# Kernel optimization log

Measured on AMD Instinct MI355X. Metric: run time of the kernel, lower is better.

Reference implementation:

```python
import jax, jax.numpy as jnp
import numpy as np

BN_EPS = 1e-5
DIST_EPS = 1e-8
K = 3  # fixed 3-NN interpolation


def _cond_conv(x, t_embed, w_t, b_t, w_c, b_c, gamma, beta):
    # time conditioning: GELU(t) -> Linear -> add to channels
    te = jax.nn.gelu(t_embed, approximate=False) @ w_t.T + b_t  # (B, Cin)
    x = x + te[:, :, None]
    # kernel-size-1 Conv1d == channel GEMM
    x = jnp.einsum('oc,bcn->bon', w_c, x) + b_c[None, :, None]
    # BatchNorm1d, training mode: biased stats over (batch, length)
    m = jnp.mean(x, axis=(0, 2), keepdims=True)
    v = jnp.var(x, axis=(0, 2), keepdims=True)
    x = gamma[None, :, None] * (x - m) * jax.lax.rsqrt(v + BN_EPS) + beta[None, :, None]
    return jax.nn.gelu(x, approximate=False)


def _forward(xyz1, xyz2, points1, points2, t_embed,
             w_t1, b_t1, w_c1, b_c1, g1, be1,
             w_t2, b_t2, w_c2, b_c2, g2, be2):
    # squared euclidean distances (cdist**2), computed directly
    # d2[b,n,s] = ||xyz1[b,n]||^2 + ||xyz2[b,s]||^2 - 2 <xyz1[b,n], xyz2[b,s]>
    n1 = jnp.sum(xyz1 * xyz1, axis=-1)  # (B,N)
    n2 = jnp.sum(xyz2 * xyz2, axis=-1)  # (B,S)
    d2 = n1[:, :, None] + n2[:, None, :] - 2.0 * jnp.einsum('bnc,bsc->bns', xyz1, xyz2)
    # top-3 smallest distances (instead of wasteful full sort)
    neg, idx = jax.lax.top_k(-d2, K)        # (B,N,3)
    dists = -neg
    dist_recip = 1.0 / (dists + DIST_EPS)
    weight = dist_recip / jnp.sum(dist_recip, axis=2, keepdims=True)  # (B,N,3)
    pts2t = jnp.transpose(points2, (0, 2, 1))  # (B,S,C2)
    gathered = jax.vmap(lambda p, i: p[i])(pts2t, idx)  # (B,N,3,C2)
    interp = jnp.einsum('bnkc,bnk->bcn', gathered, weight)  # (B,C2,N)
    new_points = jnp.concatenate([points1, interp], axis=1)  # (B,C1+C2,N)
    new_points = _cond_conv(new_points, t_embed, w_t1, b_t1, w_c1, b_c1, g1, be1)
    new_points = _cond_conv(new_points, t_embed, w_t2, b_t2, w_c2, b_c2, g2, be2)
    return new_points


def setup_inputs() -> dict:
    key = jax.random.key(0)
    ks = jax.random.split(key, 12)
    B, N, S, C1, C2, T = 8, 8192, 2048, 128, 256, 256
    Cin = C1 + C2
    s = lambda fan: 1.0 / np.sqrt(fan)
    return {
        'xyz1': jax.random.normal(ks[0], (B, N, 3), jnp.float32),
        'xyz2': jax.random.normal(ks[1], (B, S, 3), jnp.float32),
        'points1': jax.random.normal(ks[2], (B, C1, N), jnp.float32),
        'points2': jax.random.normal(ks[3], (B, C2, S), jnp.float32),
        't_embed': jax.random.normal(ks[4], (B, T), jnp.float32),
        'w_t1': jax.random.normal(ks[5], (Cin, T), jnp.float32) * s(T),
        'b_t1': jnp.zeros((Cin,), jnp.float32),
        'w_c1': jax.random.normal(ks[6], (256, Cin), jnp.float32) * s(Cin),
        'b_c1': jnp.zeros((256,), jnp.float32),
        'g1': jnp.ones((256,), jnp.float32),
        'be1': jnp.zeros((256,), jnp.float32),
        'w_t2': jax.random.normal(ks[7], (256, T), jnp.float32) * s(T),
        'b_t2': jnp.zeros((256,), jnp.float32),
        'w_c2': jax.random.normal(ks[8], (256, 256), jnp.float32) * s(256),
        'b_c2': jnp.zeros((256,), jnp.float32),
        'g2': jnp.ones((256,), jnp.float32),
        'be2': jnp.zeros((256,), jnp.float32),
    }


def reference(xyz1, xyz2, points1, points2, t_embed,
              w_t1, b_t1, w_c1, b_c1, g1, be1,
              w_t2, b_t2, w_c2, b_c2, g2, be2):
    return _forward(xyz1, xyz2, points1, points2, t_embed,
                    w_t1, b_t1, w_c1, b_c1, g1, be1,
                    w_t2, b_t2, w_c2, b_c2, g2, be2)
```

## Files before the change

kernel.cpp:

```cpp
#include <hip/hip_runtime.h>
#include <cfloat>
#include <cmath>

#define B_   8
#define N_   8192
#define S_   2048
#define C1_  128
#define C2_  256
#define T_   256
#define CIN_ 384
#define CO_  256

#define KCH  8
#define KCS  (S_ / KCH)
#define KQB  512

typedef __attribute__((ext_vector_type(8))) short short8;
typedef __attribute__((ext_vector_type(4))) float f32x4;

__device__ __forceinline__ float bf2f(unsigned short u) {
    union { unsigned int i; float f; } v; v.i = ((unsigned int)u) << 16; return v.f;
}
__device__ __forceinline__ unsigned short f2bf(float f) {
    union { float f; unsigned int i; } v; v.f = f;
    unsigned int i = v.i;
    unsigned int r = i + 0x7FFFu + ((i >> 16) & 1u);
    return (unsigned short)(r >> 16);
}
__device__ __forceinline__ float gelu_f(float x) {
    return 0.5f * x * (1.0f + erff(x * 0.70710678118654752440f));
}
__device__ __forceinline__ void async16(const void* g, void* l) {
    __builtin_amdgcn_global_load_lds((const __attribute__((address_space(1))) void*)g,
                                     (__attribute__((address_space(3))) void*)l, 16, 0, 0);
}
__device__ __forceinline__ float med3f(float a, float b, float c) {
    float r;
    asm("v_med3_f32 %0, %1, %2, %3" : "=v"(r) : "v"(a), "v"(b), "v"(c));
    return r;
}

#define OFF_TE1   0u
#define OFF_TE2   16384u
#define OFF_BN1   28672u
#define OFF_BN2   30720u
#define OFF_WC1   1605632u
#define OFF_WC2   1802240u
#define OFF_P2T   2097152u
#define OFF_X1    10485760u
#define OFF_Y     60817408u
#define OFF_PD    OFF_Y
#define OFF_PI    (OFF_Y + 6291456u)
#define OFF_PS    OFF_P2T
#define OFF_PQ    (OFF_P2T + 1048576u)

__global__ __launch_bounds__(256) void prep_kernel(
    const float* __restrict__ w1, const float* __restrict__ w2,
    unsigned short* __restrict__ o1, unsigned short* __restrict__ o2,
    const float* __restrict__ t_embed,
    const float* __restrict__ w_t1, const float* __restrict__ b_t1,
    const float* __restrict__ w_t2, const float* __restrict__ b_t2,
    float* __restrict__ te1, float* __restrict__ te2)
{
    int bx = blockIdx.x, t = threadIdx.x;
    if (bx < 384) {
        int g = bx * 256 + t;
        o1[g] = f2bf(w1[g]);
        if (g < CO_ * CO_) o2[g] = f2bf(w2[g]);
        return;
    }
    __shared__ float gt[T_];
    int b = bx - 384;
    gt[t] = gelu_f(t_embed[b * T_ + t]);
    __syncthreads();
    for (int o = t; o < CIN_ + CO_; o += 256) {
        if (o < CIN_) {
            const float* w = w_t1 + o * T_;
            float s = 0.f;
            for (int k = 0; k < T_; ++k) s += gt[k] * w[k];
            te1[b * CIN_ + o] = s + b_t1[o];
        } else {
            int oo = o - CIN_;
            const float* w = w_t2 + oo * T_;
            float s = 0.f;
            for (int k = 0; k < T_; ++k) s += gt[k] * w[k];
            te2[b * CO_ + oo] = s + b_t2[oo];
        }
    }
}

__global__ __launch_bounds__(256) void knn_part_kernel(
    const float* __restrict__ xyz1, const float* __restrict__ xyz2,
    float* __restrict__ pd, int* __restrict__ pi)
{
    __shared__ float4 sp[KCS];
    int b = blockIdx.z, ch = blockIdx.y, tid = threadIdx.x;
    int s0 = ch * KCS;
    {
        int gs = s0 + tid;
        float x = xyz2[(b * S_ + gs) * 3 + 0];
        float y = xyz2[(b * S_ + gs) * 3 + 1];
        float z = xyz2[(b * S_ + gs) * 3 + 2];
        sp[tid] = make_float4(x, y, z, x * x + y * y + z * z);
    }
    __syncthreads();

    float nx[2], ny[2], nz[2], nn[2];
    float d1[2], d2[2], d3[2];
    int   i1[2], i2[2], i3[2];
    #pragma unroll
    for (int qq = 0; qq < 2; ++qq) {
        int n = blockIdx.x * KQB + qq * 256 + tid;
        float x1 = xyz1[(b * N_ + n) * 3 + 0];
        float y1 = xyz1[(b * N_ + n) * 3 + 1];
        float z1 = xyz1[(b * N_ + n) * 3 + 2];
        nn[qq] = x1 * x1 + y1 * y1 + z1 * z1;
        nx[qq] = -2.0f * x1; ny[qq] = -2.0f * y1; nz[qq] = -2.0f * z1;
        d1[qq] = FLT_MAX; d2[qq] = FLT_MAX; d3[qq] = FLT_MAX;
        i1[qq] = 0; i2[qq] = 0; i3[qq] = 0;
    }

    for (int s = 0; s < KCS; s += 4) {
        #pragma unroll
        for (int u = 0; u < 4; ++u) {
            float4 p = sp[s + u];
            int gi = s0 + s + u;
            #pragma unroll
            for (int qq = 0; qq < 2; ++qq) {
                float d = fmaf(nx[qq], p.x,
                          fmaf(ny[qq], p.y,
                          fmaf(nz[qq], p.z, p.w)));
                bool c1 = d < d1[qq];
                bool c2 = d < d2[qq];
                bool c3 = d < d3[qq];
                float e1 = fminf(d1[qq], d);
                float e2 = med3f(d1[qq], d2[qq], d);
                float e3 = med3f(d2[qq], d3[qq], d);
                int u1  = c1 ? i1[qq] : gi;
                int n1i = c1 ? gi : i1[qq];
                int n2i = c2 ? u1 : i2[qq];
                int u2  = c2 ? i2[qq] : gi;
                int n3i = c3 ? u2 : i3[qq];
                d1[qq] = e1; d2[qq] = e2; d3[qq] = e3;
                i1[qq] = n1i; i2[qq] = n2i; i3[qq] = n3i;
            }
        }
    }

    #pragma unroll
    for (int qq = 0; qq < 2; ++qq) {
        int n = blockIdx.x * KQB + qq * 256 + tid;
        size_t pb = (((size_t)b * KCH + ch) * N_ + n) * 3;
        pd[pb + 0] = d1[qq] + nn[qq];
        pd[pb + 1] = d2[qq] + nn[qq];
        pd[pb + 2] = d3[qq] + nn[qq];
        pi[pb + 0] = i1[qq]; pi[pb + 1] = i2[qq]; pi[pb + 2] = i3[qq];
    }
}

__global__ __launch_bounds__(256) void transpose_fused(
    const float* __restrict__ p2, unsigned short* __restrict__ p2t,
    const float* __restrict__ p1, const float* __restrict__ te1,
    unsigned short* __restrict__ X1)
{
    __shared__ unsigned short tile[32][33];
    int bx = blockIdx.x;
    if (bx < 4096) {
        int b = bx >> 9, cy = (bx >> 6) & 7, sx = bx & 63;
        int s0 = sx * 32, c0 = cy * 32;
        #pragma unroll
        for (int j = 0; j < 4; ++j) {
            int c = threadIdx.y + j * 8;
            tile[c][threadIdx.x] = f2bf(p2[((size_t)b * C2_ + c0 + c) * S_ + s0 + threadIdx.x]);
        }
        __syncthreads();
        #pragma unroll
        for (int j = 0; j < 4; ++j) {
            int s = threadIdx.y + j * 8;
            p2t[((size_t)b * S_ + s0 + s) * C2_ + c0 + threadIdx.x] = tile[threadIdx.x][s];
        }
    } else {
        int bz = bx - 4096;
        int b = bz >> 10, cy = (bz >> 8) & 3, nx = bz & 255;
        int n0 = nx * 32, c0 = cy * 32;
        const float* te = te1 + b * CIN_;
        #pragma unroll
        for (int j = 0; j < 4; ++j) {
            int c = threadIdx.y + j * 8;
            tile[c][threadIdx.x] =
                f2bf(p1[((size_t)b * C1_ + c0 + c) * N_ + n0 + threadIdx.x] + te[c0 + c]);
        }
        __syncthreads();
        #pragma unroll
        for (int j = 0; j < 4; ++j) {
            int n = threadIdx.y + j * 8;
            X1[((size_t)b * N_ + n0 + n) * CIN_ + c0 + threadIdx.x] = tile[threadIdx.x][n];
        }
    }
}

__global__ __launch_bounds__(256) void interp2_kernel(
    const float* __restrict__ pd, const int* __restrict__ pi,
    const unsigned short* __restrict__ p2t,
    const float* __restrict__ te1, unsigned short* __restrict__ X1)
{
    __shared__ float spd[KCH][8][3];
    __shared__ int   spi[KCH][8][3];
    __shared__ float ste[C2_];
    int tid = threadIdx.x;
    int b = blockIdx.x >> 10;
    int n0 = (blockIdx.x & 1023) * 8;
    ste[tid] = te1[b * CIN_ + C1_ + tid];
    if (tid < 64) {
        int ch = tid >> 3, r = tid & 7;
        size_t pb = (((size_t)b * KCH + ch) * N_ + n0 + r) * 3;
        spd[ch][r][0] = pd[pb]; spd[ch][r][1] = pd[pb + 1]; spd[ch][r][2] = pd[pb + 2];
    } else if (tid < 128) {
        int t2 = tid - 64;
        int ch = t2 >> 3, r = t2 & 7;
        size_t pb = (((size_t)b * KCH + ch) * N_ + n0 + r) * 3;
        spi[ch][r][0] = pi[pb]; spi[ch][r][1] = pi[pb + 1]; spi[ch][r][2] = pi[pb + 2];
    }
    __syncthreads();

    int r = tid >> 5;
    int l = tid & 31;
    float d1, d2, d3; int i1, i2, i3;
    if (l < KCH) {
        d1 = spd[l][r][0]; d2 = spd[l][r][1]; d3 = spd[l][r][2];
        i1 = spi[l][r][0]; i2 = spi[l][r][1]; i3 = spi[l][r][2];
    } else {
        d1 = d2 = d3 = FLT_MAX;
        i1 = i2 = i3 = 0x7FFFFFFF;
    }
    #pragma unroll
    for (int m = 1; m <= 4; m <<= 1) {
        float pd1 = __shfl_xor(d1, m), pd2 = __shfl_xor(d2, m), pd3 = __shfl_xor(d3, m);
        int   pi1 = __shfl_xor(i1, m), pi2 = __shfl_xor(i2, m), pi3 = __shfl_xor(i3, m);
        #pragma unroll
        for (int k = 0; k < 3; ++k) {
            float d = (k == 0) ? pd1 : (k == 1) ? pd2 : pd3;
            int   i = (k == 0) ? pi1 : (k == 1) ? pi2 : pi3;
            bool c1 = (d < d1) || (d == d1 && i < i1);
            bool c2 = (d < d2) || (d == d2 && i < i2);
            bool c3 = (d < d3) || (d == d3 && i < i3);
            float e1 = c1 ? d : d1;        int j1 = c1 ? i : i1;
            float e2 = c1 ? d1 : (c2 ? d : d2);
            int   j2 = c1 ? i1 : (c2 ? i : i2);
            float e3 = c2 ? d2 : (c3 ? d : d3);
            int   j3 = c2 ? i2 : (c3 ? i : i3);
            d1 = e1; d2 = e2; d3 = e3; i1 = j1; i2 = j2; i3 = j3;
        }
    }
    int base = threadIdx.x & 32;
    d1 = __shfl(d1, base); d2 = __shfl(d2, base); d3 = __shfl(d3, base);
    i1 = __shfl(i1, base); i2 = __shfl(i2, base); i3 = __shfl(i3, base);
    float r1 = 1.0f / (d1 + 1e-8f);
    float r2 = 1.0f / (d2 + 1e-8f);
    float r3 = 1.0f / (d3 + 1e-8f);
    float rs = 1.0f / (r1 + r2 + r3);
    float w0 = r1 * rs, w1 = r2 * rs, w2 = r3 * rs;

    int gr = (b << 13) + n0 + r;
    int co = l * 8;
    const unsigned short* q0 = p2t + ((size_t)b * S_ + i1) * C2_ + co;
    const unsigned short* q1 = p2t + ((size_t)b * S_ + i2) * C2_ + co;
    const unsigned short* q2 = p2t + ((size_t)b * S_ + i3) * C2_ + co;
    union { short8 v; unsigned short u[8]; } a0, a1, a2, pk;
    a0.v = *(const short8*)q0;
    a1.v = *(const short8*)q1;
    a2.v = *(const short8*)q2;
    #pragma unroll
    for (int jj = 0; jj < 8; ++jj) {
        float v = w0 * bf2f(a0.u[jj]) + w1 * bf2f(a1.u[jj]) + w2 * bf2f(a2.u[jj])
                + ste[co + jj];
        pk.u[jj] = f2bf(v);
    }
    *(short8*)&X1[(size_t)gr * CIN_ + C1_ + co] = pk.v;
}

template <int K, int MODE>
__global__ __launch_bounds__(256) void gemm_bt(
    const unsigned short* __restrict__ A,
    const unsigned short* __restrict__ X,
    const float* __restrict__ bias,
    unsigned short* __restrict__ out,
    float* __restrict__ psum, float* __restrict__ psq)
{
    __shared__ unsigned short sA[128 * 64];
    __shared__ unsigned short sB[128 * 64];
    const int tid = threadIdx.x;
    const int lane = tid & 63, wave = tid >> 6;
    const int wo = wave >> 1, wm = wave & 1;
    const int quad = lane >> 4, col = lane & 15;
    const int b = blockIdx.z;
    const int x = blockIdx.x;
    const int perm = (x & 7) * 16 + (x >> 3);
    const int n_t = perm >> 1, o_t = perm & 1;
    const int o0 = o_t * 128;
    const int n0 = n_t * 128;
    const unsigned short* Xb = X + (size_t)b * N_ * K;
    const int prow = ((b << 6) + n_t) * 2 + wm;

    f32x4 acc[4][4];
    #pragma unroll
    for (int i = 0; i < 4; ++i)
        #pragma unroll
        for (int j = 0; j < 4; ++j) acc[i][j] = (f32x4){0.f, 0.f, 0.f, 0.f};

    for (int k0 = 0; k0 < K; k0 += 64) {
        #pragma unroll
        for (int i = 0; i < 4; ++i) {
            int chunk = i * 256 + tid;
            int row = chunk >> 3, c8 = chunk & 7;
            async16(&A [(o0 + row) * K + k0 + c8 * 8], &sA[chunk * 8]);
            async16(&Xb[(size_t)(n0 + row) * K + k0 + c8 * 8], &sB[chunk * 8]);
        }
        __syncthreads();
        #pragma unroll
        for (int kk = 0; kk < 64; kk += 32) {
            short8 af[4], bfr[4];
            #pragma unroll
            for (int i = 0; i < 4; ++i)
                af[i] = *(const short8*)&sA[(wo * 64 + i * 16 + col) * 64 + kk + quad * 8];
            #pragma unroll
            for (int j = 0; j < 4; ++j)
                bfr[j] = *(const short8*)&sB[(wm * 64 + j * 16 + col) * 64 + kk + quad * 8];
            #pragma unroll
            for (int i = 0; i < 4; ++i)
                #pragma unroll
                for (int j = 0; j < 4; ++j)
                    acc[i][j] = __builtin_amdgcn_mfma_f32_16x16x32_bf16(af[i], bfr[j], acc[i][j], 0, 0, 0);
        }
        __syncthreads();
    }

    #pragma unroll
    for (int i = 0; i < 4; ++i) {
        int oo = o0 + wo * 64 + i * 16 + quad * 4;
        float bv0 = bias[oo + 0], bv1 = bias[oo + 1];
        float bv2 = bias[oo + 2], bv3 = bias[oo + 3];
        float s0 = 0.f, s1 = 0.f, s2 = 0.f, s3 = 0.f;
        float q0 = 0.f, q1 = 0.f, q2 = 0.f, q3 = 0.f;
        #pragma unroll
        for (int j = 0; j < 4; ++j) {
            int nn = n0 + wm * 64 + j * 16 + col;
            float v0 = acc[i][j][0] + bv0, v1 = acc[i][j][1] + bv1;
            float v2 = acc[i][j][2] + bv2, v3 = acc[i][j][3] + bv3;
            s0 += v0; q0 += v0 * v0; s1 += v1; q1 += v1 * v1;
            s2 += v2; q2 += v2 * v2; s3 += v3; q3 += v3 * v3;
            if (MODE == 0) {
                union { unsigned short u[4]; uint2 p; } pk;
                pk.u[0] = f2bf(v0); pk.u[1] = f2bf(v1);
                pk.u[2] = f2bf(v2); pk.u[3] = f2bf(v3);
                *(uint2*)&out[((size_t)b * N_ + nn) * CO_ + oo] = pk.p;
            } else {
                out[((size_t)b * CO_ + oo + 0) * N_ + nn] = f2bf(v0);
                out[((size_t)b * CO_ + oo + 1) * N_ + nn] = f2bf(v1);
                out[((size_t)b * CO_ + oo + 2) * N_ + nn] = f2bf(v2);
                out[((size_t)b * CO_ + oo + 3) * N_ + nn] = f2bf(v3);
            }
        }
        #pragma unroll
        for (int off = 1; off < 16; off <<= 1) {
            s0 += __shfl_down(s0, off); q0 += __shfl_down(q0, off);
            s1 += __shfl_down(s1, off); q1 += __shfl_down(q1, off);
            s2 += __shfl_down(s2, off); q2 += __shfl_down(q2, off);
            s3 += __shfl_down(s3, off); q3 += __shfl_down(q3, off);
        }
        if (col == 0) {
            float* ps = psum + (size_t)oo * 1024 + prow;
            float* pq = psq  + (size_t)oo * 1024 + prow;
            ps[0] = s0; ps[1024] = s1; ps[2048] = s2; ps[3072] = s3;
            pq[0] = q0; pq[1024] = q1; pq[2048] = q2; pq[3072] = q3;
        }
    }
}

__global__ __launch_bounds__(256) void bn_reduce_kernel(
    const float* __restrict__ psum, const float* __restrict__ psq,
    const float* __restrict__ gamma, const float* __restrict__ beta,
    float* __restrict__ scale, float* __restrict__ shift)
{
    int ch = blockIdx.x * 8 + (threadIdx.x >> 5);
    int l = threadIdx.x & 31;
    float s = 0.f, q = 0.f;
    for (int r = l; r < 1024; r += 32) {
        s += psum[(size_t)ch * 1024 + r];
        q += psq [(size_t)ch * 1024 + r];
    }
    #pragma unroll
    for (int off = 16; off > 0; off >>= 1) {
        s += __shfl_down(s, off, 32);
        q += __shfl_down(q, off, 32);
    }
    if (l == 0) {
        const float inv = 1.0f / 65536.0f;
        float m = s * inv;
        float var = fmaxf(q * inv - m * m, 0.f);
        float sc = gamma[ch] / sqrtf(var + 1e-5f);
        scale[ch] = sc;
        shift[ch] = beta[ch] - m * sc;
    }
}

__global__ __launch_bounds__(256) void apply1_kernel(
    unsigned short* __restrict__ y, const float* __restrict__ scale,
    const float* __restrict__ shift, const float* __restrict__ te2)
{
    __shared__ float ssc[CO_], ssh[CO_], ste[CO_];
    int b = blockIdx.x >> 10;
    int t = threadIdx.x;
    ssc[t] = scale[t]; ssh[t] = shift[t]; ste[t] = te2[b * CO_ + t];
    __syncthreads();
    int g = blockIdx.x * 256 + t;
    int row = g >> 5;
    int og = (g & 31) * 8;
    unsigned short* p = y + (size_t)row * CO_ + og;
    union { short8 v; unsigned short u[8]; } in, op;
    in.v = *(short8*)p;
    #pragma unroll
    for (int jj = 0; jj < 8; ++jj) {
        int o = og + jj;
        op.u[jj] = f2bf(gelu_f(ssc[o] * bf2f(in.u[jj]) + ssh[o]) + ste[o]);
    }
    *(short8*)p = op.v;
}

__global__ __launch_bounds__(256) void final_kernel(
    const unsigned short* __restrict__ z, const float* __restrict__ scale,
    const float* __restrict__ shift, float* __restrict__ out)
{
    int g = blockIdx.x * 256 + threadIdx.x;
    size_t e = (size_t)g * 8;
    int row = (int)(e >> 13);
    int o = row & (CO_ - 1);
    float sc = scale[o], sh = shift[o];
    union { short8 v; unsigned short u[8]; } in;
    in.v = *(const short8*)&z[e];
    float vo[8];
    #pragma unroll
    for (int jj = 0; jj < 8; ++jj)
        vo[jj] = gelu_f(sc * bf2f(in.u[jj]) + sh);
    *(float4*)&out[e]     = make_float4(vo[0], vo[1], vo[2], vo[3]);
    *(float4*)&out[e + 4] = make_float4(vo[4], vo[5], vo[6], vo[7]);
}

extern "C" void kernel_launch(void* const* d_in, const int* in_sizes, int n_in,
                              void* d_out, int out_size, void* d_ws, size_t ws_size,
                              hipStream_t stream)
{
    (void)in_sizes; (void)n_in; (void)out_size; (void)ws_size;
    const float* xyz1    = (const float*)d_in[0];
    const float* xyz2    = (const float*)d_in[1];
    const float* points1 = (const float*)d_in[2];
    const float* points2 = (const float*)d_in[3];
    const float* t_embed = (const float*)d_in[4];
    const float* w_t1    = (const float*)d_in[5];
    const float* b_t1    = (const float*)d_in[6];
    const float* w_c1    = (const float*)d_in[7];
    const float* b_c1    = (const float*)d_in[8];
    const float* g1      = (const float*)d_in[9];
    const float* be1     = (const float*)d_in[10];
    const float* w_t2    = (const float*)d_in[11];
    const float* b_t2    = (const float*)d_in[12];
    const float* w_c2    = (const float*)d_in[13];
    const float* b_c2    = (const float*)d_in[14];
    const float* g2      = (const float*)d_in[15];
    const float* be2     = (const float*)d_in[16];

    char* w = (char*)d_ws;
    float* te1        = (float*)(w + OFF_TE1);
    float* te2        = (float*)(w + OFF_TE2);
    float* scale1     = (float*)(w + OFF_BN1);
    float* shift1     = scale1 + 256;
    float* scale2     = (float*)(w + OFF_BN2);
    float* shift2     = scale2 + 256;
    unsigned short* wc1 = (unsigned short*)(w + OFF_WC1);
    unsigned short* wc2 = (unsigned short*)(w + OFF_WC2);
    unsigned short* p2t = (unsigned short*)(w + OFF_P2T);
    float* pd         = (float*)(w + OFF_PD);
    int*   pi         = (int*)(w + OFF_PI);
    float* psum       = (float*)(w + OFF_PS);
    float* psq        = (float*)(w + OFF_PQ);
    unsigned short* X1  = (unsigned short*)(w + OFF_X1);
    unsigned short* Z   = (unsigned short*)(w + OFF_X1);
    unsigned short* Y   = (unsigned short*)(w + OFF_Y);
    float* out = (float*)d_out;

    hipLaunchKernelGGL(prep_kernel, dim3(392), dim3(256), 0, stream,
                       w_c1, w_c2, wc1, wc2, t_embed, w_t1, b_t1, w_t2, b_t2, te1, te2);
    hipLaunchKernelGGL(knn_part_kernel, dim3(N_ / KQB, KCH, B_), dim3(256), 0, stream,
                       xyz1, xyz2, pd, pi);
    hipLaunchKernelGGL(transpose_fused, dim3(12288), dim3(32, 8), 0, stream,
                       points2, p2t, points1, te1, X1);
    hipLaunchKernelGGL(interp2_kernel, dim3(B_ * N_ / 8), dim3(256), 0, stream,
                       pd, pi, p2t, te1, X1);
    hipLaunchKernelGGL((gemm_bt<CIN_, 0>), dim3(128, 1, B_), dim3(256), 0, stream,
                       wc1, X1, b_c1, Y, psum, psq);
    hipLaunchKernelGGL(bn_reduce_kernel, dim3(32), dim3(256), 0, stream,
                       psum, psq, g1, be1, scale1, shift1);
    hipLaunchKernelGGL(apply1_kernel, dim3(8192), dim3(256), 0, stream,
                       Y, scale1, shift1, te2);
    hipLaunchKernelGGL((gemm_bt<CO_, 1>), dim3(128, 1, B_), dim3(256), 0, stream,
                       wc2, Y, b_c2, Z, psum, psq);
    hipLaunchKernelGGL(bn_reduce_kernel, dim3(32), dim3(256), 0, stream,
                       psum, psq, g2, be2, scale2, shift2);
    hipLaunchKernelGGL(final_kernel, dim3(8192), dim3(256), 0, stream,
                       Z, scale2, shift2, out);
}
```

Baseline: 355.9 us.

## Merge launches into two mega-kernels and replace BN reduce with atomics

After: 498.3 us. 1.4x slower.

```diff
diff --git a/kernel.cpp b/kernel.cpp
--- a/kernel.cpp
+++ b/kernel.cpp
@@ -42,8 +42,7 @@
 
 #define OFF_TE1   0u
 #define OFF_TE2   16384u
-#define OFF_BN1   28672u
-#define OFF_BN2   30720u
+#define OFF_ST    32768u
 #define OFF_WC1   1605632u
 #define OFF_WC2   1802240u
 #define OFF_P2T   2097152u
@@ -51,232 +50,238 @@
 #define OFF_Y     60817408u
 #define OFF_PD    OFF_Y
 #define OFF_PI    (OFF_Y + 6291456u)
-#define OFF_PS    OFF_P2T
-#define OFF_PQ    (OFF_P2T + 1048576u)
-
-__global__ __launch_bounds__(256) void prep_kernel(
+
+__global__ __launch_bounds__(256) void mega1_kernel(
+    const float* __restrict__ xyz1, const float* __restrict__ xyz2,
+    float* __restrict__ pd, int* __restrict__ pi,
     const float* __restrict__ w1, const float* __restrict__ w2,
     unsigned short* __restrict__ o1, unsigned short* __restrict__ o2,
     const float* __restrict__ t_embed,
     const float* __restrict__ w_t1, const float* __restrict__ b_t1,
     const float* __restrict__ w_t2, const float* __restrict__ b_t2,
-    float* __restrict__ te1, float* __restrict__ te2)
+    float* __restrict__ te1, float* __restrict__ te2,
+    const float* __restrict__ p2, unsigned short* __restrict__ p2t,
+    float* __restrict__ stats)
 {
-    int bx = blockIdx.x, t = threadIdx.x;
-    if (bx < 384) {
-        int g = bx * 256 + t;
-        o1[g] = f2bf(w1[g]);
-        if (g < CO_ * CO_) o2[g] = f2bf(w2[g]);
-        return;
+    __shared__ __align__(16) char smem[4096];
+    int bx = blockIdx.x, tid = threadIdx.x;
+
+    if (bx < 1024) {
+        float4* sp = (float4*)smem;
+        int x = bx & 15, ch = (bx >> 4) & 7, b = bx >> 7;
+        int s0 = ch * KCS;
+        {
+            int gs = s0 + tid;
+            float xx = xyz2[(b * S_ + gs) * 3 + 0];
+            float yy = xyz2[(b * S_ + gs) * 3 + 1];
+            float zz = xyz2[(b * S_ + gs) * 3 + 2];
+            sp[tid] = make_float4(xx, yy, zz, xx * xx + yy * yy + zz * zz);
+        }
+        __syncthreads();
+
+        float nx[2], ny[2], nz[2], nn[2];
+        float d1[2], d2[2], d3[2];
+        int   i1[2], i2[2], i3[2];
+        #pragma unroll
+        for (int qq = 0; qq < 2; ++qq) {
+            int n = x * KQB + qq * 256 + tid;
+            float x1 = xyz1[(b * N_ + n) * 3 + 0];
+            float y1 = xyz1[(b * N_ + n) * 3 + 1];
+            float z1 = xyz1[(b * N_ + n) * 3 + 2];
+            nn[qq] = x1 * x1 + y1 * y1 + z1 * z1;
+            nx[qq] = -2.0f * x1; ny[qq] = -2.0f * y1; nz[qq] = -2.0f * z1;
+            d1[qq] = FLT_MAX; d2[qq] = FLT_MAX; d3[qq] = FLT_MAX;
+            i1[qq] = 0; i2[qq] = 0; i3[qq] = 0;
+        }
+
+        for (int s = 0; s < KCS; s += 4) {
+            #pragma unroll
+            for (int u = 0; u < 4; ++u) {
+                float4 p = sp[s + u];
+                int gi = s0 + s + u;
+                #pragma unroll
+                for (int qq = 0; qq < 2; ++qq) {
+                    float d = fmaf(nx[qq], p.x,
+                              fmaf(ny[qq], p.y,
+                              fmaf(nz[qq], p.z, p.w)));
+                    bool c1 = d < d1[qq];
+                    bool c2 = d < d2[qq];
+                    bool c3 = d < d3[qq];
+                    float e1 = fminf(d1[qq], d);
+                    float e2 = med3f(d1[qq], d2[qq], d);
+                    float e3 = med3f(d2[qq], d3[qq], d);
+                    int u1  = c1 ? i1[qq] : gi;
+                    int n1i = c1 ? gi : i1[qq];
+                    int n2i = c2 ? u1 : i2[qq];
+                    int u2  = c2 ? i2[qq] : gi;
+                    int n3i = c3 ? u2 : i3[qq];
+                    d1[qq] = e1; d2[qq] = e2; d3[qq] = e3;
+                    i1[qq] = n1i; i2[qq] = n2i; i3[qq] = n3i;
+                }
+            }
+        }
+
+        #pragma unroll
+        for (int qq = 0; qq < 2; ++qq) {
+            int n = x * KQB + qq * 256 + tid;
+            size_t pb = (((size_t)b * KCH + ch) * N_ + n) * 3;
+            pd[pb + 0] = d1[qq] + nn[qq];
+            pd[pb + 1] = d2[qq] + nn[qq];
+            pd[pb + 2] = d3[qq] + nn[qq];
+            pi[pb + 0] = i1[qq]; pi[pb + 1] = i2[qq]; pi[pb + 2] = i3[qq];
+        }
+    } else if (bx < 1416) {
+        int pbx = bx - 1024;
+        if (pbx < 384) {
+            int g = pbx * 256 + tid;
+            o1[g] = f2bf(w1[g]);
+            if (g < CO_ * CO_) o2[g] = f2bf(w2[g]);
+            return;
+        }
+        float* gt = (float*)smem;
+        int b = pbx - 384;
+        gt[tid] = gelu_f(t_embed[b * T_ + tid]);
+        __syncthreads();
+        for (int o = tid; o < CIN_ + CO_; o += 256) {
+            if (o < CIN_) {
+                const float* w = w_t1 + o * T_;
+                float s = 0.f;
+                for (int k = 0; k < T_; ++k) s += gt[k] * w[k];
+                te1[b * CIN_ + o] = s + b_t1[o];
+            } else {
+                int oo = o - CIN_;
+                const float* w = w_t2 + oo * T_;
+                float s = 0.f;
+                for (int k = 0; k < T_; ++k) s += gt[k] * w[k];
+                te2[b * CO_ + oo] = s + b_t2[oo];
+            }
+        }
+    } else if (bx < 5512) {
+        unsigned short (*tile)[33] = (unsigned short (*)[33])smem;
+        int bz = bx - 1416;
+        int b = bz >> 9, cy = (bz >> 6) & 7, sx = bz & 63;
+        int s0 = sx * 32, c0 = cy * 32;
+        int tx = tid & 31, ty = tid >> 5;
+        #pragma unroll
+        for (int j = 0; j < 4; ++j) {
+            int c = ty + j * 8;
+            tile[c][tx] = f2bf(p2[((size_t)b * C2_ + c0 + c) * S_ + s0 + tx]);
+        }
+        __syncthreads();
+        #pragma unroll
+        for (int j = 0; j < 4; ++j) {
+            int s = ty + j * 8;
+            p2t[((size_t)b * S_ + s0 + s) * C2_ + c0 + tx] = tile[tx][s];
+        }
+    } else {
+        stats[tid] = 0.f; stats[tid + 256] = 0.f;
+        stats[tid + 512] = 0.f; stats[tid + 768] = 0.f;
     }
-    __shared__ float gt[T_];
-    int b = bx - 384;
-    gt[t] = gelu_f(t_embed[b * T_ + t]);
-    __syncthreads();
-    for (int o = t; o < CIN_ + CO_; o += 256) {
-        if (o < CIN_) {
-            const float* w = w_t1 + o * T_;
-            float s = 0.f;
-            for (int k = 0; k < T_; ++k) s += gt[k] * w[k];
-            te1[b * CIN_ + o] = s + b_t1[o];
-        } else {
-            int oo = o - CIN_;
-            const float* w = w_t2 + oo * T_;
-            float s = 0.f;
-            for (int k = 0; k < T_; ++k) s += gt[k] * w[k];
-            te2[b * CO_ + oo] = s + b_t2[oo];
-        }
-    }
-}
-
-__global__ __launch_bounds__(256) void knn_part_kernel(
-    const float* __restrict__ xyz1, const float* __restrict__ xyz2,
-    float* __restrict__ pd, int* __restrict__ pi)
-{
-    __shared__ float4 sp[KCS];
-    int b = blockIdx.z, ch = blockIdx.y, tid = threadIdx.x;
-    int s0 = ch * KCS;
-    {
-        int gs = s0 + tid;
-        float x = xyz2[(b * S_ + gs) * 3 + 0];
-        float y = xyz2[(b * S_ + gs) * 3 + 1];
-        float z = xyz2[(b * S_ + gs) * 3 + 2];
-        sp[tid] = make_float4(x, y, z, x * x + y * y + z * z);
-    }
-    __syncthreads();
-
-    float nx[2], ny[2], nz[2], nn[2];
-    float d1[2], d2[2], d3[2];
-    int   i1[2], i2[2], i3[2];
-    #pragma unroll
-    for (int qq = 0; qq < 2; ++qq) {
-        int n = blockIdx.x * KQB + qq * 256 + tid;
-        float x1 = xyz1[(b * N_ + n) * 3 + 0];
-        float y1 = xyz1[(b * N_ + n) * 3 + 1];
-        float z1 = xyz1[(b * N_ + n) * 3 + 2];
-        nn[qq] = x1 * x1 + y1 * y1 + z1 * z1;
-        nx[qq] = -2.0f * x1; ny[qq] = -2.0f * y1; nz[qq] = -2.0f * z1;
-        d1[qq] = FLT_MAX; d2[qq] = FLT_MAX; d3[qq] = FLT_MAX;
-        i1[qq] = 0; i2[qq] = 0; i3[qq] = 0;
-    }
-
-    for (int s = 0; s < KCS; s += 4) {
-        #pragma unroll
-        for (int u = 0; u < 4; ++u) {
-            float4 p = sp[s + u];
-            int gi = s0 + s + u;
-            #pragma unroll
-            for (int qq = 0; qq < 2; ++qq) {
-                float d = fmaf(nx[qq], p.x,
-                          fmaf(ny[qq], p.y,
-                          fmaf(nz[qq], p.z, p.w)));
-                bool c1 = d < d1[qq];
-                bool c2 = d < d2[qq];
-                bool c3 = d < d3[qq];
-                float e1 = fminf(d1[qq], d);
-                float e2 = med3f(d1[qq], d2[qq], d);
-                float e3 = med3f(d2[qq], d3[qq], d);
-                int u1  = c1 ? i1[qq] : gi;
-                int n1i = c1 ? gi : i1[qq];
-                int n2i = c2 ? u1 : i2[qq];
-                int u2  = c2 ? i2[qq] : gi;
-                int n3i = c3 ? u2 : i3[qq];
-                d1[qq] = e1; d2[qq] = e2; d3[qq] = e3;
-                i1[qq] = n1i; i2[qq] = n2i; i3[qq] = n3i;
-            }
-        }
-    }
-
-    #pragma unroll
-    for (int qq = 0; qq < 2; ++qq) {
-        int n = blockIdx.x * KQB + qq * 256 + tid;
-        size_t pb = (((size_t)b * KCH + ch) * N_ + n) * 3;
-        pd[pb + 0] = d1[qq] + nn[qq];
-        pd[pb + 1] = d2[qq] + nn[qq];
-        pd[pb + 2] = d3[qq] + nn[qq];
-        pi[pb + 0] = i1[qq]; pi[pb + 1] = i2[qq]; pi[pb + 2] = i3[qq];
-    }
-}
-
-__global__ __launch_bounds__(256) void transpose_fused(
-    const float* __restrict__ p2, unsigned short* __restrict__ p2t,
-    const float* __restrict__ p1, const float* __restrict__ te1,
+}
+
+__global__ __launch_bounds__(256) void mega2_kernel(
+    const float* __restrict__ pd, const int* __restrict__ pi,
+    const unsigned short* __restrict__ p2t,
+    const float* __restrict__ te1,
+    const float* __restrict__ p1,
     unsigned short* __restrict__ X1)
 {
-    __shared__ unsigned short tile[32][33];
-    int bx = blockIdx.x;
-    if (bx < 4096) {
-        int b = bx >> 9, cy = (bx >> 6) & 7, sx = bx & 63;
-        int s0 = sx * 32, c0 = cy * 32;
-        #pragma unroll
-        for (int j = 0; j < 4; ++j) {
-            int c = threadIdx.y + j * 8;
-            tile[c][threadIdx.x] = f2bf(p2[((size_t)b * C2_ + c0 + c) * S_ + s0 + threadIdx.x]);
-        }
-        __syncthreads();
-        #pragma unroll
-        for (int j = 0; j < 4; ++j) {
-            int s = threadIdx.y + j * 8;
-            p2t[((size_t)b * S_ + s0 + s) * C2_ + c0 + threadIdx.x] = tile[threadIdx.x][s];
-        }
+    __shared__ __align__(16) char smem[4096];
+    int bx = blockIdx.x, tid = threadIdx.x;
+
+    if (bx < 8192) {
+        float (*spd)[8][3] = (float (*)[8][3])smem;
+        int   (*spi)[8][3] = (int (*)[8][3])(smem + 768);
+        float* ste = (float*)(smem + 1536);
+        int b = bx >> 10;
+        int n0 = (bx & 1023) * 8;
+        ste[tid] = te1[b * CIN_ + C1_ + tid];
+        if (tid < 64) {
+            int ch = tid >> 3, r = tid & 7;
+            size_t pb = (((size_t)b * KCH + ch) * N_ + n0 + r) * 3;
+            spd[ch][r][0] = pd[pb]; spd[ch][r][1] = pd[pb + 1]; spd[ch][r][2] = pd[pb + 2];
+        } else if (tid < 128) {
+            int t2 = tid - 64;
+            int ch = t2 >> 3, r = t2 & 7;
+            size_t pb = (((size_t)b * KCH + ch) * N_ + n0 + r) * 3;
+            spi[ch][r][0] = pi[pb]; spi[ch][r][1] = pi[pb + 1]; spi[ch][r][2] = pi[pb + 2];
+        }
+        __syncthreads();
+
+        int r = tid >> 5;
+        int l = tid & 31;
+        float d1, d2, d3; int i1, i2, i3;
+        if (l < KCH) {
+            d1 = spd[l][r][0]; d2 = spd[l][r][1]; d3 = spd[l][r][2];
+            i1 = spi[l][r][0]; i2 = spi[l][r][1]; i3 = spi[l][r][2];
+        } else {
+            d1 = d2 = d3 = FLT_MAX;
+            i1 = i2 = i3 = 0x7FFFFFFF;
+        }
+        #pragma unroll
+        for (int m = 1; m <= 4; m <<= 1) {
+            float pd1 = __shfl_xor(d1, m), pd2 = __shfl_xor(d2, m), pd3 = __shfl_xor(d3, m);
+            int   pi1 = __shfl_xor(i1, m), pi2 = __shfl_xor(i2, m), pi3 = __shfl_xor(i3, m);
+            #pragma unroll
+            for (int k = 0; k < 3; ++k) {
+                float d = (k == 0) ? pd1 : (k == 1) ? pd2 : pd3;
+                int   i = (k == 0) ? pi1 : (k == 1) ? pi2 : pi3;
+                bool c1 = (d < d1) || (d == d1 && i < i1);
+                bool c2 = (d < d2) || (d == d2 && i < i2);
+                bool c3 = (d < d3) || (d == d3 && i < i3);
+                float e1 = c1 ? d : d1;        int j1 = c1 ? i : i1;
+                float e2 = c1 ? d1 : (c2 ? d : d2);
+                int   j2 = c1 ? i1 : (c2 ? i : i2);
+                float e3 = c2 ? d2 : (c3 ? d : d3);
+                int   j3 = c2 ? i2 : (c3 ? i : i3);
+                d1 = e1; d2 = e2; d3 = e3; i1 = j1; i2 = j2; i3 = j3;
+            }
+        }
+        int base = tid & 32;
+        d1 = __shfl(d1, base); d2 = __shfl(d2, base); d3 = __shfl(d3, base);
+        i1 = __shfl(i1, base); i2 = __shfl(i2, base); i3 = __shfl(i3, base);
+        float r1 = 1.0f / (d1 + 1e-8f);
+        float r2 = 1.0f / (d2 + 1e-8f);
+        float r3 = 1.0f / (d3 + 1e-8f);
+        float rs = 1.0f / (r1 + r2 + r3);
+        float w0 = r1 * rs, w1 = r2 * rs, w2 = r3 * rs;
+
+        int gr = (b << 13) + n0 + r;
+        int co = l * 8;
+        const unsigned short* q0 = p2t + ((size_t)b * S_ + i1) * C2_ + co;
+        const unsigned short* q1 = p2t + ((size_t)b * S_ + i2) * C2_ + co;
+        const unsigned short* q2 = p2t + ((size_t)b * S_ + i3) * C2_ + co;
+        union { short8 v; unsigned short u[8]; } a0, a1, a2, pk;
+        a0.v = *(const short8*)q0;
+        a1.v = *(const short8*)q1;
+        a2.v = *(const short8*)q2;
+        #pragma unroll
+        for (int jj = 0; jj < 8; ++jj) {
+            float v = w0 * bf2f(a0.u[jj]) + w1 * bf2f(a1.u[jj]) + w2 * bf2f(a2.u[jj])
+                    + ste[co + jj];
+            pk.u[jj] = f2bf(v);
+        }
+        *(short8*)&X1[(size_t)gr * CIN_ + C1_ + co] = pk.v;
     } else {
-        int bz = bx - 4096;
+        unsigned short (*tile)[33] = (unsigned short (*)[33])smem;
+        int bz = bx - 8192;
         int b = bz >> 10, cy = (bz >> 8) & 3, nx = bz & 255;
         int n0 = nx * 32, c0 = cy * 32;
+        int tx = tid & 31, ty = tid >> 5;
         const float* te = te1 + b * CIN_;
         #pragma unroll
         for (int j = 0; j < 4; ++j) {
-            int c = threadIdx.y + j * 8;
-            tile[c][threadIdx.x] =
-                f2bf(p1[((size_t)b * C1_ + c0 + c) * N_ + n0 + threadIdx.x] + te[c0 + c]);
+            int c = ty + j * 8;
+            tile[c][tx] =
+                f2bf(p1[((size_t)b * C1_ + c0 + c) * N_ + n0 + tx] + te[c0 + c]);
         }
         __syncthreads();
         #pragma unroll
         for (int j = 0; j < 4; ++j) {
-            int n = threadIdx.y + j * 8;
-            X1[((size_t)b * N_ + n0 + n) * CIN_ + c0 + threadIdx.x] = tile[threadIdx.x][n];
+            int n = ty + j * 8;
+            X1[((size_t)b * N_ + n0 + n) * CIN_ + c0 + tx] = tile[tx][n];
         }
     }
-}
-
-__global__ __launch_bounds__(256) void interp2_kernel(
-    const float* __restrict__ pd, const int* __restrict__ pi,
-    const unsigned short* __restrict__ p2t,
-    const float* __restrict__ te1, unsigned short* __restrict__ X1)
-{
-    __shared__ float spd[KCH][8][3];
-    __shared__ int   spi[KCH][8][3];
-    __shared__ float ste[C2_];
-    int tid = threadIdx.x;
-    int b = blockIdx.x >> 10;
-    int n0 = (blockIdx.x & 1023) * 8;
-    ste[tid] = te1[b * CIN_ + C1_ + tid];
-    if (tid < 64) {
-        int ch = tid >> 3, r = tid & 7;
-        size_t pb = (((size_t)b * KCH + ch) * N_ + n0 + r) * 3;
-        spd[ch][r][0] = pd[pb]; spd[ch][r][1] = pd[pb + 1]; spd[ch][r][2] = pd[pb + 2];
-    } else if (tid < 128) {
-        int t2 = tid - 64;
-        int ch = t2 >> 3, r = t2 & 7;
-        size_t pb = (((size_t)b * KCH + ch) * N_ + n0 + r) * 3;
-        spi[ch][r][0] = pi[pb]; spi[ch][r][1] = pi[pb + 1]; spi[ch][r][2] = pi[pb + 2];
-    }
-    __syncthreads();
-
-    int r = tid >> 5;
-    int l = tid & 31;
-    float d1, d2, d3; int i1, i2, i3;
-    if (l < KCH) {
-        d1 = spd[l][r][0]; d2 = spd[l][r][1]; d3 = spd[l][r][2];
-        i1 = spi[l][r][0]; i2 = spi[l][r][1]; i3 = spi[l][r][2];
-    } else {
-        d1 = d2 = d3 = FLT_MAX;
-        i1 = i2 = i3 = 0x7FFFFFFF;
-    }
-    #pragma unroll
-    for (int m = 1; m <= 4; m <<= 1) {
-        float pd1 = __shfl_xor(d1, m), pd2 = __shfl_xor(d2, m), pd3 = __shfl_xor(d3, m);
-        int   pi1 = __shfl_xor(i1, m), pi2 = __shfl_xor(i2, m), pi3 = __shfl_xor(i3, m);
-        #pragma unroll
-        for (int k = 0; k < 3; ++k) {
-            float d = (k == 0) ? pd1 : (k == 1) ? pd2 : pd3;
-            int   i = (k == 0) ? pi1 : (k == 1) ? pi2 : pi3;
-            bool c1 = (d < d1) || (d == d1 && i < i1);
-            bool c2 = (d < d2) || (d == d2 && i < i2);
-            bool c3 = (d < d3) || (d == d3 && i < i3);
-            float e1 = c1 ? d : d1;        int j1 = c1 ? i : i1;
-            float e2 = c1 ? d1 : (c2 ? d : d2);
-            int   j2 = c1 ? i1 : (c2 ? i : i2);
-            float e3 = c2 ? d2 : (c3 ? d : d3);
-            int   j3 = c2 ? i2 : (c3 ? i : i3);
-            d1 = e1; d2 = e2; d3 = e3; i1 = j1; i2 = j2; i3 = j3;
-        }
-    }
-    int base = threadIdx.x & 32;
-    d1 = __shfl(d1, base); d2 = __shfl(d2, base); d3 = __shfl(d3, base);
-    i1 = __shfl(i1, base); i2 = __shfl(i2, base); i3 = __shfl(i3, base);
-    float r1 = 1.0f / (d1 + 1e-8f);
-    float r2 = 1.0f / (d2 + 1e-8f);
-    float r3 = 1.0f / (d3 + 1e-8f);
-    float rs = 1.0f / (r1 + r2 + r3);
-    float w0 = r1 * rs, w1 = r2 * rs, w2 = r3 * rs;
-
-    int gr = (b << 13) + n0 + r;
-    int co = l * 8;
-    const unsigned short* q0 = p2t + ((size_t)b * S_ + i1) * C2_ + co;
-    const unsigned short* q1 = p2t + ((size_t)b * S_ + i2) * C2_ + co;
-    const unsigned short* q2 = p2t + ((size_t)b * S_ + i3) * C2_ + co;
-    union { short8 v; unsigned short u[8]; } a0, a1, a2, pk;
-    a0.v = *(const short8*)q0;
-    a1.v = *(const short8*)q1;
-    a2.v = *(const short8*)q2;
-    #pragma unroll
-    for (int jj = 0; jj < 8; ++jj) {
-        float v = w0 * bf2f(a0.u[jj]) + w1 * bf2f(a1.u[jj]) + w2 * bf2f(a2.u[jj])
-                + ste[co + jj];
-        pk.u[jj] = f2bf(v);
-    }
-    *(short8*)&X1[(size_t)gr * CIN_ + C1_ + co] = pk.v;
 }
 
 template <int K, int MODE>
@@ -300,7 +305,6 @@
     const int o0 = o_t * 128;
     const int n0 = n_t * 128;
     const unsigned short* Xb = X + (size_t)b * N_ * K;
-    const int prow = ((b << 6) + n_t) * 2 + wm;
 
     f32x4 acc[4][4];
     #pragma unroll
@@ -369,49 +373,33 @@
             s3 += __shfl_down(s3, off); q3 += __shfl_down(q3, off);
         }
         if (col == 0) {
-            float* ps = psum + (size_t)oo * 1024 + prow;
-            float* pq = psq  + (size_t)oo * 1024 + prow;
-            ps[0] = s0; ps[1024] = s1; ps[2048] = s2; ps[3072] = s3;
-            pq[0] = q0; pq[1024] = q1; pq[2048] = q2; pq[3072] = q3;
+            atomicAdd(&psum[oo + 0], s0); atomicAdd(&psum[oo + 1], s1);
+            atomicAdd(&psum[oo + 2], s2); atomicAdd(&psum[oo + 3], s3);
+            atomicAdd(&psq[oo + 0], q0); atomicAdd(&psq[oo + 1], q1);
+            atomicAdd(&psq[oo + 2], q2); atomicAdd(&psq[oo + 3], q3);
         }
     }
 }
 
-__global__ __launch_bounds__(256) void bn_reduce_kernel(
+__global__ __launch_bounds__(256) void apply1_kernel(
+    unsigned short* __restrict__ y,
     const float* __restrict__ psum, const float* __restrict__ psq,
     const float* __restrict__ gamma, const float* __restrict__ beta,
-    float* __restrict__ scale, float* __restrict__ shift)
-{
-    int ch = blockIdx.x * 8 + (threadIdx.x >> 5);
-    int l = threadIdx.x & 31;
-    float s = 0.f, q = 0.f;
-    for (int r = l; r < 1024; r += 32) {
-        s += psum[(size_t)ch * 1024 + r];
-        q += psq [(size_t)ch * 1024 + r];
-    }
-    #pragma unroll
-    for (int off = 16; off > 0; off >>= 1) {
-        s += __shfl_down(s, off, 32);
-        q += __shfl_down(q, off, 32);
-    }
-    if (l == 0) {
-        const float inv = 1.0f / 65536.0f;
-        float m = s * inv;
-        float var = fmaxf(q * inv - m * m, 0.f);
-        float sc = gamma[ch] / sqrtf(var + 1e-5f);
-        scale[ch] = sc;
-        shift[ch] = beta[ch] - m * sc;
-    }
-}
-
-__global__ __launch_bounds__(256) void apply1_kernel(
-    unsigned short* __restrict__ y, const float* __restrict__ scale,
-    const float* __restrict__ shift, const float* __restrict__ te2)
+    const float* __restrict__ te2)
 {
     __shared__ float ssc[CO_], ssh[CO_], ste[CO_];
     int b = blockIdx.x >> 10;
     int t = threadIdx.x;
-    ssc[t] = scale[t]; ssh[t] = shift[t]; ste[t] = te2[b * CO_ + t];
+    {
+        const float inv = 1.0f / 65536.0f;
+        float s = psum[t], q = psq[t];
+        float m = s * inv;
+        float var = fmaxf(q * inv - m * m, 0.f);
+        float sc = gamma[t] / sqrtf(var + 1e-5f);
+        ssc[t] = sc;
+        ssh[t] = beta[t] - m * sc;
+        ste[t] = te2[b * CO_ + t];
+    }
     __syncthreads();
     int g = blockIdx.x * 256 + t;
     int row = g >> 5;
@@ -428,14 +416,22 @@
 }
 
 __global__ __launch_bounds__(256) void final_kernel(
-    const unsigned short* __restrict__ z, const float* __restrict__ scale,
-    const float* __restrict__ shift, float* __restrict__ out)
+    const unsigned short* __restrict__ z,
+    const float* __restrict__ psum, const float* __restrict__ psq,
+    const float* __restrict__ gamma, const float* __restrict__ beta,
+    float* __restrict__ out)
 {
-    int g = blockIdx.x * 256 + threadIdx.x;
+    int bx = blockIdx.x;
+    int o = (bx >> 2) & (CO_ - 1);
+    const float inv = 1.0f / 65536.0f;
+    float s = psum[o], q = psq[o];
+    float m = s * inv;
+    float var = fmaxf(q * inv - m * m, 0.f);
+    float sc = gamma[o] / sqrtf(var + 1e-5f);
+    float sh = beta[o] - m * sc;
+
+    int g = bx * 256 + threadIdx.x;
     size_t e = (size_t)g * 8;
-    int row = (int)(e >> 13);
-    int o = row & (CO_ - 1);
-    float sc = scale[o], sh = shift[o];
     union { short8 v; unsigned short u[8]; } in;
     in.v = *(const short8*)&z[e];
     float vo[8];
@@ -472,40 +468,34 @@
     char* w = (char*)d_ws;
     float* te1        = (float*)(w + OFF_TE1);
     float* te2        = (float*)(w + OFF_TE2);
-    float* scale1     = (float*)(w + OFF_BN1);
-    float* shift1     = scale1 + 256;
-    float* scale2     = (float*)(w + OFF_BN2);
-    float* shift2     = scale2 + 256;
+    float* stats      = (float*)(w + OFF_ST);
+    float* psum1      = stats;
+    float* psq1       = stats + 256;
+    float* psum2      = stats + 512;
+    float* psq2       = stats + 768;
     unsigned short* wc1 = (unsigned short*)(w + OFF_WC1);
     unsigned short* wc2 = (unsigned short*)(w + OFF_WC2);
     unsigned short* p2t = (unsigned short*)(w + OFF_P2T);
     float* pd         = (float*)(w + OFF_PD);
     int*   pi         = (int*)(w + OFF_PI);
-    float* psum       = (float*)(w + OFF_PS);
-    float* psq        = (float*)(w + OFF_PQ);
     unsigned short* X1  = (unsigned short*)(w + OFF_X1);
     unsigned short* Z   = (unsigned short*)(w + OFF_X1);
     unsigned short* Y   = (unsigned short*)(w + OFF_Y);
     float* out = (float*)d_out;
 
-    hipLaunchKernelGGL(prep_kernel, dim3(392), dim3(256), 0, stream,
-                       w_c1, w_c2, wc1, wc2, t_embed, w_t1, b_t1, w_t2, b_t2, te1, te2);
-    hipLaunchKernelGGL(knn_part_kernel, dim3(N_ / KQB, KCH, B_), dim3(256), 0, stream,
-                       xyz1, xyz2, pd, pi);
-    hipLaunchKernelGGL(transpose_fused, dim3(12288), dim3(32, 8), 0, stream,
-                       points2, p2t, points1, te1, X1);
-    hipLaunchKernelGGL(interp2_kernel, dim3(B_ * N_ / 8), dim3(256), 0, stream,
-                       pd, pi, p2t, te1, X1);
+    hipLaunchKernelGGL(mega1_kernel, dim3(5513), dim3(256), 0, stream,
+                       xyz1, xyz2, pd, pi,
+                       w_c1, w_c2, wc1, wc2,
+                       t_embed, w_t1, b_t1, w_t2, b_t2, te1, te2,
+                       points2, p2t, stats);
+    hipLaunchKernelGGL(mega2_kernel, dim3(16384), dim3(256), 0, stream,
+                       pd, pi, p2t, te1, points1, X1);
     hipLaunchKernelGGL((gemm_bt<CIN_, 0>), dim3(128, 1, B_), dim3(256), 0, stream,
-                       wc1, X1, b_c1, Y, psum, psq);
-    hipLaunchKernelGGL(bn_reduce_kernel, dim3(32), dim3(256), 0, stream,
-                       psum, psq, g1, be1, scale1, shift1);
+                       wc1, X1, b_c1, Y, psum1, psq1);
     hipLaunchKernelGGL(apply1_kernel, dim3(8192), dim3(256), 0, stream,
-                       Y, scale1, shift1, te2);
+                       Y, psum1, psq1, g1, be1, te2);
     hipLaunchKernelGGL((gemm_bt<CO_, 1>), dim3(128, 1, B_), dim3(256), 0, stream,
-                       wc2, Y, b_c2, Z, psum, psq);
-    hipLaunchKernelGGL(bn_reduce_kernel, dim3(32), dim3(256), 0, stream,
-                       psum, psq, g2, be2, scale2, shift2);
+                       wc2, Y, b_c2, Z, psum2, psq2);
     hipLaunchKernelGGL(final_kernel, dim3(8192), dim3(256), 0, stream,
-                       Z, scale2, shift2, out);
-}
+                       Z, psum2, psq2, g2, be2, out);
+}
```
